# Optimization experiments

Measured on AMD Instinct MI355X. Metric: run time of the kernel, lower is better.

The kernel has to match this reference:

```python
import jax, jax.numpy as jnp
import numpy as np

HIDDEN = 768
FF = 3072
N_HEADS = 12
HEAD = HIDDEN // N_HEADS
WIDTH = 512  # attention window (number of attended keys, causal)
B, S = 2, 4096
EPS = 1e-6


def _rotary_sincos(seq_len, dim):
    # GPT-J style: freqs per pair, each value repeated twice (interleaved)
    inv_freq = 1.0 / (10000.0 ** (np.arange(0, dim, 2, dtype=np.float32) / dim))
    t = np.arange(seq_len, dtype=np.float32)
    ang = np.einsum('s,d->sd', t, inv_freq)              # [S, dim/2]
    ang = np.repeat(ang, 2, axis=-1)                     # [S, dim]
    return jnp.asarray(np.sin(ang))[:, None, :], jnp.asarray(np.cos(ang))[:, None, :]


def setup_inputs() -> dict:
    key = jax.random.key(0)
    ks = jax.random.split(key, 4)
    x = jax.random.normal(ks[0], (B, S, HIDDEN), dtype=jnp.float32)
    sin, cos = _rotary_sincos(S, HEAD)                   # [S,1,HEAD] each
    W_in = jax.random.normal(ks[1], (HIDDEN, 3 * HIDDEN + FF), dtype=jnp.float32) / np.sqrt(HIDDEN)
    b_in = jnp.zeros((3 * HIDDEN + FF,), dtype=jnp.float32)
    W_out = jax.random.normal(ks[2], (HIDDEN + FF, HIDDEN), dtype=jnp.float32) / np.sqrt(HIDDEN + FF)
    b_out = jnp.zeros((HIDDEN,), dtype=jnp.float32)
    w_norm = jnp.ones((HIDDEN,), dtype=jnp.float32)
    return {"x": x, "sin": sin, "cos": cos, "w_norm": w_norm,
            "W_in": W_in, "b_in": b_in, "W_out": W_out, "b_out": b_out}


def _rotate_every_two(x):
    x1 = x[..., ::2]
    x2 = x[..., 1::2]
    return jnp.stack((-x2, x1), axis=-1).reshape(x.shape)


def _apply_rope(x, sin, cos):
    # x: [B,S,H,hd]; sin/cos: [S,1,hd] -> broadcast as [1,S,1,hd]
    sin = sin[None]
    cos = cos[None]
    return x * cos + _rotate_every_two(x) * sin


def _windowed_attention(q, k, v, width):
    # q,k,v: [B,S,H,hd]; causal local attention: key j valid iff 0 <= i-j < width
    b, s, h, d = q.shape
    wb = width  # block size == window; each query block attends blocks (b-1, b)
    nb = s // wb
    scale = 1.0 / np.sqrt(d)
    qb = q.reshape(b, nb, wb, h, d)
    kp = jnp.pad(k, ((0, 0), (wb, 0), (0, 0), (0, 0))).reshape(b, nb + 1, wb, h, d)
    vp = jnp.pad(v, ((0, 0), (wb, 0), (0, 0), (0, 0))).reshape(b, nb + 1, wb, h, d)
    kb = jnp.concatenate([kp[:, :-1], kp[:, 1:]], axis=2)   # [B,nb,2wb,H,hd]
    vb = jnp.concatenate([vp[:, :-1], vp[:, 1:]], axis=2)
    scores = jnp.einsum('bnqhd,bnkhd->bnhqk', qb, kb) * scale
    qi = jnp.arange(wb)
    ki = jnp.arange(2 * wb)
    bi = jnp.arange(nb)
    diff = wb + qi[:, None] - ki[None, :]                    # i - j per block
    base = (diff >= 0) & (diff < width)                      # [wb, 2wb]
    valid_j = (bi[:, None, None] >= 1) | (ki[None, None, :] >= wb)  # j >= 0
    mask = base[None] & valid_j                              # [nb, wb, 2wb]
    neg = jnp.finfo(scores.dtype).min
    scores = jnp.where(mask[None, :, None], scores, neg)
    p = jax.nn.softmax(scores, axis=-1)
    out = jnp.einsum('bnhqk,bnkhd->bnqhd', p, vb)
    return out.reshape(b, s, h * d)


def reference(x, sin, cos, w_norm, W_in, b_in, W_out, b_out):
    # RMSNorm
    ms = jnp.mean(x * x, axis=-1, keepdims=True)
    xn = x * jax.lax.rsqrt(ms + EPS) * w_norm
    # fused QKV + FF projection
    t = xn @ W_in + b_in                                     # [B,S,3*HIDDEN+FF]
    ff = t[:, :, -FF:]
    qkv = t[:, :, :-FF].reshape(x.shape[0], x.shape[1], 3, N_HEADS, HEAD)
    q = _apply_rope(qkv[:, :, 0], sin, cos)
    k = _apply_rope(qkv[:, :, 1], sin, cos)
    v = qkv[:, :, 2]
    attn = _windowed_attention(q, k, v, WIDTH)               # [B,S,HIDDEN]
    ff = jax.nn.gelu(ff, approximate=False)
    combined = jnp.concatenate((attn, ff), axis=-1)          # [B,S,HIDDEN+FF]
    return combined @ W_out + b_out
```

## Files before the change

kernel.cpp:

```cpp
#include <hip/hip_runtime.h>
#include <hip/hip_bf16.h>

typedef short bf16x8 __attribute__((ext_vector_type(8)));
typedef float f32x4 __attribute__((ext_vector_type(4)));

#define LOG2E 1.4426950408889634f
#define QKV_E ((size_t)24*4096*64)

__device__ __forceinline__ float bfu2f(unsigned short u) {
  unsigned v = ((unsigned)u) << 16;
  return __builtin_bit_cast(float, v);
}
__device__ __forceinline__ unsigned short f2bfu(float f) {
  unsigned u = __builtin_bit_cast(unsigned, f);
  u += 0x7fffu + ((u >> 16) & 1u);
  return (unsigned short)(u >> 16);
}
__device__ __forceinline__ unsigned packbf2(float lo, float hi) {
  return (unsigned)f2bfu(lo) | ((unsigned)f2bfu(hi) << 16);
}
__device__ __forceinline__ float gelu_f(float v) {
  float a = fabsf(v) * 0.70710678118654752f;
  float t = 1.0f / (1.0f + 0.3275911f * a);
  float poly = ((((1.061405429f * t - 1.453152027f) * t + 1.421413741f) * t
                 - 0.284496736f) * t + 0.254829592f) * t;
  float erfa = 1.0f - poly * __expf(-a * a);
  float erfv = v >= 0.0f ? erfa : -erfa;
  return 0.5f * v * (1.0f + erfv);
}
__device__ __forceinline__ void gl_lds16(const ushort* g, ushort* l) {
  __builtin_amdgcn_global_load_lds(
      (const __attribute__((address_space(1))) unsigned int*)(const void*)g,
      (__attribute__((address_space(3))) unsigned int*)(void*)l, 16, 0, 0);
}
#define WAIT_VM8  asm volatile("s_waitcnt vmcnt(8)" ::: "memory")
#define WAIT_VM2  asm volatile("s_waitcnt vmcnt(2)" ::: "memory")
#define WAIT_VM0  asm volatile("s_waitcnt vmcnt(0)" ::: "memory")
#define WAIT_LGKM asm volatile("s_waitcnt lgkmcnt(0)" ::: "memory")
#define BAR       __builtin_amdgcn_s_barrier()

__global__ __launch_bounds__(256) void rmsnorm_k(const float* __restrict__ x,
    const float* __restrict__ w, ushort* __restrict__ xn) {
  int row = blockIdx.x, t = threadIdx.x;
  const float* xr = x + (size_t)row * 768;
  float v0 = xr[t], v1 = xr[t + 256], v2 = xr[t + 512];
  float ss = v0 * v0 + v1 * v1 + v2 * v2;
#pragma unroll
  for (int m = 32; m >= 1; m >>= 1) ss += __shfl_xor(ss, m, 64);
  __shared__ float part[4];
  if ((t & 63) == 0) part[t >> 6] = ss;
  __syncthreads();
  float tot = part[0] + part[1] + part[2] + part[3];
  float rr = rsqrtf(tot * (1.0f / 768.0f) + 1e-6f);
  ushort* xo = xn + (size_t)row * 768;
  xo[t]       = f2bfu(v0 * rr * w[t]);
  xo[t + 256] = f2bfu(v1 * rr * w[t + 256]);
  xo[t + 512] = f2bfu(v2 * rr * w[t + 512]);
}

__global__ __launch_bounds__(256) void tcvt_k(const float* __restrict__ in,
    ushort* __restrict__ out, int R, int C) {
  __shared__ float tile[32][33];
  int c0 = blockIdx.x * 32, r0 = blockIdx.y * 32;
  int t = threadIdx.x;
  int j = t & 31, i0 = t >> 5;
#pragma unroll
  for (int i = i0; i < 32; i += 8) tile[i][j] = in[(size_t)(r0 + i) * C + c0 + j];
  __syncthreads();
#pragma unroll
  for (int i = i0; i < 32; i += 8) out[(size_t)(c0 + i) * R + r0 + j] = f2bfu(tile[j][i]);
}

__global__ __launch_bounds__(512, 2) void gemm1_k(const ushort* __restrict__ A,
    const ushort* __restrict__ Bt, const float* __restrict__ bias,
    const float* __restrict__ sn, const float* __restrict__ cs,
    ushort* __restrict__ qbuf, ushort* __restrict__ kbuf,
    ushort* __restrict__ vt, ushort* __restrict__ comb) {
  __shared__ __align__(16) ushort lds[2][32768];
  const int t = threadIdx.x, lane = t & 63, w = t >> 6;
  const int wm = w >> 2, wn = w & 3;
  const int g = lane >> 4, q15 = lane & 15;
  int bid = blockIdx.x;
  int xcd = bid & 7, local = bid >> 3;
  int grp = local / 28, r28 = local % 28;
  int bx = grp * 7 + r28 % 7;
  int by = xcd * 4 + r28 / 7;
  const int mBase = by * 256, nBase = bx * 256;

  const int schk = ((t & 7) ^ ((t >> 3) & 7)) * 8;
  const ushort* gA = A  + (size_t)(mBase + (t >> 3)) * 768 + schk;
  const ushort* gB = Bt + (size_t)(nBase + (t >> 3)) * 768 + schk;
  const int dstBase = w * 512;

  f32x4 acc[8][4];
  f32x4 z = {0.f, 0.f, 0.f, 0.f};
#pragma unroll
  for (int mi = 0; mi < 8; ++mi)
#pragma unroll
    for (int nj = 0; nj < 4; ++nj) acc[mi][nj] = z;

#pragma unroll
  for (int rd = 0; rd < 4; ++rd) {
    gl_lds16(gA + rd * 49152, &lds[0][rd * 4096 + dstBase]);
    gl_lds16(gB + rd * 49152, &lds[0][16384 + rd * 4096 + dstBase]);
  }

#pragma unroll 1
  for (int kt = 0; kt < 12; ++kt) {
    const int cur = kt & 1;
    const ushort* As = &lds[cur][0];
    const ushort* Bs = &lds[cur][16384];
    bf16x8 bff[4];
#pragma unroll
    for (int p = 0; p < 4; ++p) {
      if (kt < 11) {
        const int k1 = (kt + 1) * 64;
        const int r0 = 2 * p, r1 = 2 * p + 1;
        if (r0 < 4) gl_lds16(gA + r0 * 49152 + k1, &lds[1 - cur][r0 * 4096 + dstBase]);
        else        gl_lds16(gB + (r0 - 4) * 49152 + k1, &lds[1 - cur][16384 + (r0 - 4) * 4096 + dstBase]);
        if (r1 < 4) gl_lds16(gA + r1 * 49152 + k1, &lds[1 - cur][r1 * 4096 + dstBase]);
        else        gl_lds16(gB + (r1 - 4) * 49152 + k1, &lds[1 - cur][16384 + (r1 - 4) * 4096 + dstBase]);
      }
      if (p == 0) {
        if (kt < 11) { WAIT_VM2; } else { WAIT_VM0; }
        BAR;
      }
      const int kk = p >> 1, mih = p & 1;
      if (mih == 0) {
#pragma unroll
        for (int nj = 0; nj < 4; ++nj) {
          int rl = wn * 64 + nj * 16 + q15;
          bff[nj] = *(const bf16x8*)(Bs + rl * 64 + (((kk * 4 + g) ^ (q15 & 7)) << 3));
        }
      }
      bf16x8 af[4];
#pragma unroll
      for (int i = 0; i < 4; ++i) {
        int rl = wm * 128 + (mih * 4 + i) * 16 + q15;
        af[i] = *(const bf16x8*)(As + rl * 64 + (((kk * 4 + g) ^ (q15 & 7)) << 3));
      }
      BAR;
      __builtin_amdgcn_s_setprio(1);
#pragma unroll
      for (int i = 0; i < 4; ++i)
#pragma unroll
        for (int nj = 0; nj < 4; ++nj)
          acc[mih * 4 + i][nj] = __builtin_amdgcn_mfma_f32_16x16x32_bf16(
              bff[nj], af[i], acc[mih * 4 + i][nj], 0, 0, 0);
      __builtin_amdgcn_s_setprio(0);
      WAIT_LGKM;
      BAR;
    }
  }

  const int colB = nBase + wn * 64;
  const bool isff = (colB >= 2304);
  const int region = colB / 768;
#pragma unroll
  for (int mi = 0; mi < 8; ++mi) {
    int row = mBase + wm * 128 + mi * 16 + q15;
    int b = row >> 12, s = row & 4095;
#pragma unroll
    for (int nj = 0; nj < 4; ++nj) {
      int col = colB + nj * 16 + g * 4;
      f32x4 v = acc[mi][nj] + *(const f32x4*)(bias + col);
      if (isff) {
        ushort4 o;
        o.x = f2bfu(gelu_f(v[0]));
        o.y = f2bfu(gelu_f(v[1]));
        o.z = f2bfu(gelu_f(v[2]));
        o.w = f2bfu(gelu_f(v[3]));
        *(ushort4*)(comb + (size_t)row * 3840 + (col - 1536)) = o;
      } else {
        int rem = col - region * 768;
        int h = rem >> 6, d0 = rem & 63;
        if (region == 2) {
          int l = s & 127;
          int pnn = l >> 4, pg = (l >> 2) & 3, pr = l & 3;
          int sp = (s & ~127) | (((pnn >> 1) * 4 + pg) * 8 + (pnn & 1) * 4 + pr);
          size_t vb = (size_t)((b * 12 + h) * 64 + d0) * 4096 + sp;
          vt[vb]          = f2bfu(v[0]);
          vt[vb + 4096]   = f2bfu(v[1]);
          vt[vb + 2*4096] = f2bfu(v[2]);
          vt[vb + 3*4096] = f2bfu(v[3]);
        } else {
          f32x4 sv = *(const f32x4*)(sn + (s << 6) + d0);
          f32x4 cv = *(const f32x4*)(cs + (s << 6) + d0);
          float o0 = v[0] * cv[0] - v[1] * sv[0];
          float o1 = v[1] * cv[0] + v[0] * sv[0];
          float o2 = v[2] * cv[2] - v[3] * sv[2];
          float o3 = v[3] * cv[2] + v[2] * sv[2];
          ushort4 o;
          if (region == 0) {
            o.x = f2bfu(o0 * 0.125f); o.y = f2bfu(o1 * 0.125f);
            o.z = f2bfu(o2 * 0.125f); o.w = f2bfu(o3 * 0.125f);
            *(ushort4*)(qbuf + ((size_t)((b * 12 + h) * 4096 + s)) * 64 + d0) = o;
          } else {
            o.x = f2bfu(o0); o.y = f2bfu(o1); o.z = f2bfu(o2); o.w = f2bfu(o3);
            *(ushort4*)(kbuf + ((size_t)((b * 12 + h) * 4096 + s)) * 64 + d0) = o;
          }
        }
      }
    }
  }
}

__global__ __launch_bounds__(256, 2) void gemm2_k(const ushort* __restrict__ A,
    const ushort* __restrict__ Bt, const float* __restrict__ bias,
    float* __restrict__ out) {
  __shared__ __align__(16) ushort lds[2][2][128 * 64];
  const int t = threadIdx.x, lane = t & 63, w = t >> 6;
  const int wr = w >> 1, wc = w & 1;
  int bid = blockIdx.x;
  int xcd = bid & 7, local = bid >> 3;
  int g = local / 4, r4 = local % 4;
  int bx = (g % 3) * 2 + (r4 & 1);
  int by = xcd * 8 + (g / 3) * 2 + (r4 >> 1);
  const int mBase = by * 128, nBase = bx * 128;

  size_t gA[4], gB[4];
  int ldst[4];
#pragma unroll
  for (int j = 0; j < 4; ++j) {
    int row = w * 32 + j * 8 + (lane >> 3);
    int gc = ((lane & 7) ^ (lane >> 3)) * 8;
    gA[j] = (size_t)(mBase + row) * 3840 + gc;
    gB[j] = (size_t)(nBase + row) * 3840 + gc;
    ldst[j] = (w * 32 + j * 8) * 64;
  }

  f32x4 acc[4][4];
  f32x4 z = {0.f, 0.f, 0.f, 0.f};
#pragma unroll
  for (int m = 0; m < 4; ++m)
#pragma unroll
    for (int nn = 0; nn < 4; ++nn) acc[m][nn] = z;

#pragma unroll
  for (int j = 0; j < 4; ++j) {
    gl_lds16(A + gA[j], &lds[0][0][0] + ldst[j]);
    gl_lds16(Bt + gB[j], &lds[0][1][0] + ldst[j]);
  }

#pragma unroll 1
  for (int kt = 0; kt < 60; ++kt) {
    const int cur = kt & 1;
    if (kt < 59) {
      int k0 = (kt + 1) * 64;
#pragma unroll
      for (int j = 0; j < 4; ++j) {
        gl_lds16(A + gA[j] + k0, &lds[1 - cur][0][0] + ldst[j]);
        gl_lds16(Bt + gB[j] + k0, &lds[1 - cur][1][0] + ldst[j]);
      }
      WAIT_VM8;
    } else {
      WAIT_VM0;
    }
    BAR;
    const ushort* As = &lds[cur][0][0];
    const ushort* Bs = &lds[cur][1][0];
#pragma unroll
    for (int kk = 0; kk < 2; ++kk) {
      bf16x8 af[4], bff[4];
#pragma unroll
      for (int m = 0; m < 4; ++m) {
        int row = wr * 64 + m * 16 + (lane & 15);
        int slot = (kk * 4 + (lane >> 4)) ^ (lane & 7);
        af[m] = *(const bf16x8*)(As + row * 64 + slot * 8);
      }
#pragma unroll
      for (int nn = 0; nn < 4; ++nn) {
        int row = wc * 64 + nn * 16 + (lane & 15);
        int slot = (kk * 4 + (lane >> 4)) ^ (lane & 7);
        bff[nn] = *(const bf16x8*)(Bs + row * 64 + slot * 8);
      }
#pragma unroll
      for (int m = 0; m < 4; ++m)
#pragma unroll
        for (int nn = 0; nn < 4; ++nn)
          acc[m][nn] = __builtin_amdgcn_mfma_f32_16x16x32_bf16(bff[nn], af[m], acc[m][nn], 0, 0, 0);
    }
    WAIT_LGKM;
    BAR;
  }

#pragma unroll
  for (int m = 0; m < 4; ++m) {
    int row = mBase + wr * 64 + m * 16 + (lane & 15);
#pragma unroll
    for (int nn = 0; nn < 4; ++nn) {
      int col = nBase + wc * 64 + nn * 16 + ((lane >> 4) << 2);
      f32x4 v = acc[m][nn] + *(const f32x4*)(bias + col);
      *(f32x4*)(out + (size_t)row * 768 + col) = v;
    }
  }
}

__global__ __launch_bounds__(256, 2) void attn_k(const ushort* __restrict__ qb,
    const ushort* __restrict__ kb, const ushort* __restrict__ vt,
    ushort* __restrict__ comb) {
  __shared__ __align__(16) ushort KS[2][128 * 64];
  __shared__ __align__(16) ushort VS[2][64 * 128];
  int bid = blockIdx.x;
  int nb = (bid & 7) * 96 + (bid >> 3);
  int qt = nb & 31, bh = nb >> 5;
  const int t = threadIdx.x, lane = t & 63, w = t >> 6;
  const int g = lane >> 4, q15 = lane & 15;
  const int qlo = qt * 128;
  const size_t base = (size_t)bh * 4096 * 64;

  size_t kSrc[4], vSrc[4];
  int dstOff[4];
#pragma unroll
  for (int j = 0; j < 4; ++j) {
    int ck = (w * 4 + j) * 64 + lane;
    int key = ck >> 3, sl = ck & 7;
    kSrc[j] = (size_t)key * 64 + ((sl ^ (key & 7)) << 3);
    int dd = ck >> 4, s16 = ck & 15;
    vSrc[j] = (size_t)dd * 4096 + ((s16 ^ (dd & 15)) << 3);
    dstOff[j] = (w * 4 + j) * 512;
  }

  bf16x8 qa[2][2];
#pragma unroll
  for (int m = 0; m < 2; ++m)
#pragma unroll
    for (int kk = 0; kk < 2; ++kk) {
      int row = qlo + w * 32 + m * 16 + q15;
      qa[m][kk] = *(const bf16x8*)(qb + base + (size_t)row * 64 + kk * 32 + g * 8);
    }

  f32x4 z = {0.f, 0.f, 0.f, 0.f};
  f32x4 o[2][4];
#pragma unroll
  for (int m = 0; m < 2; ++m)
#pragma unroll
    for (int df = 0; df < 4; ++df) o[m][df] = z;
  float m_run[2] = {-1e30f, -1e30f}, l_run[2] = {0.f, 0.f};

  const int t0 = qt >= 4 ? qt - 4 : 0;
  const int nt = qt - t0 + 1;
  {
    int k0 = t0 * 128;
#pragma unroll
    for (int j = 0; j < 4; ++j) {
      gl_lds16(kb + base + (size_t)k0 * 64 + kSrc[j], &KS[0][0] + dstOff[j]);
      gl_lds16(vt + base + k0 + vSrc[j], &VS[0][0] + dstOff[j]);
    }
  }

  const int qrow0 = qlo + w * 32 + q15;
#pragma unroll 1
  for (int it = 0; it < nt; ++it) {
    const int kt = t0 + it, k0 = kt * 128, cur = it & 1;
    if (it + 1 < nt) {
      int k1 = k0 + 128;
#pragma unroll
      for (int j = 0; j < 4; ++j) {
        gl_lds16(kb + base + (size_t)k1 * 64 + kSrc[j], &KS[1 - cur][0] + dstOff[j]);
        gl_lds16(vt + base + k1 + vSrc[j], &VS[1 - cur][0] + dstOff[j]);
      }
      WAIT_VM8;
    } else {
      WAIT_VM0;
    }
    BAR;
    f32x4 s[2][8];
#pragma unroll
    for (int m = 0; m < 2; ++m)
#pragma unroll
      for (int nn = 0; nn < 8; ++nn) s[m][nn] = z;
#pragma unroll
    for (int kk = 0; kk < 2; ++kk) {
      bf16x8 kf[8];
#pragma unroll
      for (int nn = 0; nn < 8; ++nn) {
        int row = nn * 16 + q15;
        int slot = (kk * 4 + g) ^ (q15 & 7);
        kf[nn] = *(const bf16x8*)(&KS[cur][0] + row * 64 + slot * 8);
      }
#pragma unroll
      for (int m = 0; m < 2; ++m)
#pragma unroll
        for (int nn = 0; nn < 8; ++nn)
          s[m][nn] = __builtin_amdgcn_mfma_f32_16x16x32_bf16(kf[nn], qa[m][kk], s[m][nn], 0, 0, 0);
    }
    if (kt == qt) {
#pragma unroll
      for (int m = 0; m < 2; ++m) {
        int ql = qrow0 + m * 16 - k0;
#pragma unroll
        for (int nn = 0; nn < 8; ++nn)
#pragma unroll
          for (int r = 0; r < 4; ++r)
            if (nn * 16 + g * 4 + r > ql) s[m][nn][r] = -3e38f;
      }
    } else if (kt == qt - 4) {
#pragma unroll
      for (int m = 0; m < 2; ++m) {
        int ql = qrow0 + m * 16 - k0;
#pragma unroll
        for (int nn = 0; nn < 8; ++nn)
#pragma unroll
          for (int r = 0; r < 4; ++r)
            if (ql - (nn * 16 + g * 4 + r) >= 512) s[m][nn][r] = -3e38f;
      }
    }
    float mx[2];
    bool need = false;
#pragma unroll
    for (int m = 0; m < 2; ++m) {
      float v = s[m][0][0];
#pragma unroll
      for (int nn = 0; nn < 8; ++nn)
#pragma unroll
        for (int r = 0; r < 4; ++r) v = fmaxf(v, s[m][nn][r]);
      v = fmaxf(v, __shfl_xor(v, 16, 64));
      v = fmaxf(v, __shfl_xor(v, 32, 64));
      mx[m] = v;
      need |= (v > m_run[m] + 8.f);
    }
    if (__any(need)) {
#pragma unroll
      for (int m = 0; m < 2; ++m) {
        float mn = fmaxf(m_run[m], mx[m]);
        float sc = exp2f((m_run[m] - mn) * LOG2E);
        m_run[m] = mn;
        l_run[m] *= sc;
#pragma unroll
        for (int df = 0; df < 4; ++df) o[m][df] *= sc;
      }
    }
#pragma unroll
    for (int m = 0; m < 2; ++m) {
      float mr = m_run[m];
      float ls = 0.f;
#pragma unroll
      for (int nn = 0; nn < 8; ++nn)
#pragma unroll
        for (int r = 0; r < 4; ++r) {
          float p = exp2f((s[m][nn][r] - mr) * LOG2E);
          s[m][nn][r] = p;
          ls += p;
        }
      ls += __shfl_xor(ls, 16, 64);
      ls += __shfl_xor(ls, 32, 64);
      l_run[m] += ls;
    }
#pragma unroll
    for (int kk2 = 0; kk2 < 4; ++kk2) {
      bf16x8 pa[2];
#pragma unroll
      for (int m = 0; m < 2; ++m) {
        int4 pi4;
        pi4.x = (int)packbf2(s[m][2*kk2][0],   s[m][2*kk2][1]);
        pi4.y = (int)packbf2(s[m][2*kk2][2],   s[m][2*kk2][3]);
        pi4.z = (int)packbf2(s[m][2*kk2+1][0], s[m][2*kk2+1][1]);
        pi4.w = (int)packbf2(s[m][2*kk2+1][2], s[m][2*kk2+1][3]);
        pa[m] = __builtin_bit_cast(bf16x8, pi4);
      }
#pragma unroll
      for (int df = 0; df < 4; ++df) {
        int row = df * 16 + q15;
        int slot = (kk2 * 4 + g) ^ q15;
        bf16x8 vf = *(const bf16x8*)(&VS[cur][0] + row * 128 + slot * 8);
#pragma unroll
        for (int m = 0; m < 2; ++m)
          o[m][df] = __builtin_amdgcn_mfma_f32_16x16x32_bf16(vf, pa[m], o[m][df], 0, 0, 0);
      }
    }
    WAIT_LGKM;
    BAR;
  }

  int b = bh / 12, h = bh % 12;
#pragma unroll
  for (int m = 0; m < 2; ++m) {
    float inv = 1.0f / l_run[m];
    int row = qrow0 + m * 16;
#pragma unroll
    for (int df = 0; df < 4; ++df) {
      ushort4 ov;
      ov.x = f2bfu(o[m][df][0] * inv);
      ov.y = f2bfu(o[m][df][1] * inv);
      ov.z = f2bfu(o[m][df][2] * inv);
      ov.w = f2bfu(o[m][df][3] * inv);
      *(ushort4*)(comb + (size_t)(b * 4096 + row) * 3840 + h * 64 + df * 16 + g * 4) = ov;
    }
  }
}

extern "C" void kernel_launch(void* const* d_in, const int* in_sizes, int n_in,
                              void* d_out, int out_size, void* d_ws, size_t ws_size,
                              hipStream_t stream) {
  (void)in_sizes; (void)n_in; (void)out_size; (void)ws_size;
  const float* x      = (const float*)d_in[0];
  const float* sin_t  = (const float*)d_in[1];
  const float* cos_t  = (const float*)d_in[2];
  const float* w_norm = (const float*)d_in[3];
  const float* W_in   = (const float*)d_in[4];
  const float* b_in   = (const float*)d_in[5];
  const float* W_out  = (const float*)d_in[6];
  const float* b_out  = (const float*)d_in[7];
  float* out = (float*)d_out;

  const size_t XN_E  = (size_t)8192 * 768;
  ushort* xn      = (ushort*)d_ws;
  ushort* qbuf    = xn + XN_E;
  ushort* kbuf    = qbuf + QKV_E;
  ushort* vt      = kbuf + QKV_E;
  ushort* w_in_t  = vt + QKV_E;
  ushort* w_out_t = w_in_t + (size_t)5376 * 768;
  ushort* comb    = w_out_t + (size_t)768 * 3840;

  rmsnorm_k<<<dim3(8192), dim3(256), 0, stream>>>(x, w_norm, xn);
  tcvt_k<<<dim3(5376 / 32, 768 / 32), dim3(256), 0, stream>>>(W_in, w_in_t, 768, 5376);
  tcvt_k<<<dim3(768 / 32, 3840 / 32), dim3(256), 0, stream>>>(W_out, w_out_t, 3840, 768);
  gemm1_k<<<dim3(672), dim3(512), 0, stream>>>(xn, w_in_t, b_in, sin_t, cos_t,
                                               qbuf, kbuf, vt, comb);
  attn_k<<<dim3(768), dim3(256), 0, stream>>>(qbuf, kbuf, vt, comb);
  gemm2_k<<<dim3(384), dim3(256), 0, stream>>>(comb, w_out_t, b_out, out);
}
```

Before: 234.8 us.

## Reorder per-phase global-to-LDS prefetch so input GEMM waits only for needed rows

The input-projection GEMM now issues its next-tile B rows first, then A rows, in an order that matches when each phase consumes them. The vmcnt wait moves to the end of each phase instead of a single wait at the start of each k-tile. The prologue fully drains its loads, and the LDS-read wait is placed before the MFMA block behind a sched_barrier. The goal is to overlap more of the global-to-LDS traffic with MFMA work. In exchange, correctness depends on the exact row-to-phase mapping, and the kernel adds a barrier and wait in every phase.

```diff
diff --git a/kernel.cpp b/kernel.cpp
--- a/kernel.cpp
+++ b/kernel.cpp
@@ -101,45 +101,51 @@
 
 #pragma unroll
   for (int rd = 0; rd < 4; ++rd) {
+    gl_lds16(gB + rd * 49152, &lds[0][16384 + rd * 4096 + dstBase]);
     gl_lds16(gA + rd * 49152, &lds[0][rd * 4096 + dstBase]);
-    gl_lds16(gB + rd * 49152, &lds[0][16384 + rd * 4096 + dstBase]);
-  }
+  }
+  WAIT_VM0;
+  BAR;
 
 #pragma unroll 1
   for (int kt = 0; kt < 12; ++kt) {
     const int cur = kt & 1;
     const ushort* As = &lds[cur][0];
     const ushort* Bs = &lds[cur][16384];
+    ushort* nb = &lds[1 - cur][0];
     bf16x8 bff[4];
 #pragma unroll
     for (int p = 0; p < 4; ++p) {
       if (kt < 11) {
         const int k1 = (kt + 1) * 64;
-        const int r0 = 2 * p, r1 = 2 * p + 1;
-        if (r0 < 4) gl_lds16(gA + r0 * 49152 + k1, &lds[1 - cur][r0 * 4096 + dstBase]);
-        else        gl_lds16(gB + (r0 - 4) * 49152 + k1, &lds[1 - cur][16384 + (r0 - 4) * 4096 + dstBase]);
-        if (r1 < 4) gl_lds16(gA + r1 * 49152 + k1, &lds[1 - cur][r1 * 4096 + dstBase]);
-        else        gl_lds16(gB + (r1 - 4) * 49152 + k1, &lds[1 - cur][16384 + (r1 - 4) * 4096 + dstBase]);
-      }
-      if (p == 0) {
-        if (kt < 11) { WAIT_VM2; } else { WAIT_VM0; }
-        BAR;
+        if (p == 0) {
+          gl_lds16(gB + k1,               nb + 16384 + dstBase);
+          gl_lds16(gB + 49152 + k1,       nb + 16384 + 4096 + dstBase);
+        } else if (p == 1) {
+          gl_lds16(gB + 2 * 49152 + k1,   nb + 16384 + 2 * 4096 + dstBase);
+          gl_lds16(gB + 3 * 49152 + k1,   nb + 16384 + 3 * 4096 + dstBase);
+        } else if (p == 2) {
+          gl_lds16(gA + k1,               nb + dstBase);
+          gl_lds16(gA + 2 * 49152 + k1,   nb + 2 * 4096 + dstBase);
+        } else {
+          gl_lds16(gA + 49152 + k1,       nb + 4096 + dstBase);
+          gl_lds16(gA + 3 * 49152 + k1,   nb + 3 * 4096 + dstBase);
+        }
       }
       const int kk = p >> 1, mih = p & 1;
+      const int slot = ((kk * 4 + g) ^ (q15 & 7)) << 3;
       if (mih == 0) {
 #pragma unroll
-        for (int nj = 0; nj < 4; ++nj) {
-          int rl = wn * 64 + nj * 16 + q15;
-          bff[nj] = *(const bf16x8*)(Bs + rl * 64 + (((kk * 4 + g) ^ (q15 & 7)) << 3));
-        }
+        for (int nj = 0; nj < 4; ++nj)
+          bff[nj] = *(const bf16x8*)(Bs + (wn * 64 + nj * 16 + q15) * 64 + slot);
       }
       bf16x8 af[4];
 #pragma unroll
-      for (int i = 0; i < 4; ++i) {
-        int rl = wm * 128 + (mih * 4 + i) * 16 + q15;
-        af[i] = *(const bf16x8*)(As + rl * 64 + (((kk * 4 + g) ^ (q15 & 7)) << 3));
-      }
+      for (int i = 0; i < 4; ++i)
+        af[i] = *(const bf16x8*)(As + (wm * 128 + (mih * 4 + i) * 16 + q15) * 64 + slot);
       BAR;
+      WAIT_LGKM;
+      __builtin_amdgcn_sched_barrier(0);
       __builtin_amdgcn_s_setprio(1);
 #pragma unroll
       for (int i = 0; i < 4; ++i)
@@ -148,7 +154,7 @@
           acc[mih * 4 + i][nj] = __builtin_amdgcn_mfma_f32_16x16x32_bf16(
               bff[nj], af[i], acc[mih * 4 + i][nj], 0, 0, 0);
       __builtin_amdgcn_s_setprio(0);
-      WAIT_LGKM;
+      if (kt < 11) { WAIT_VM2; } else { WAIT_VM0; }
       BAR;
     }
   }
```

After: 239.4 us. No clear change (+2.0%).
